# Optimization experiments

Measured on AMD Instinct MI355X. Metric: run time of the kernel, lower is better.

Reference implementation:

```python
import jax, jax.numpy as jnp
import numpy as np

EPS = 1e-6
START, END, FACTOR = 2.0, 8.0, 0.5


def layer_norm(x, w, b):
    mu = jnp.mean(x, axis=-1, keepdims=True)
    var = jnp.mean(jnp.square(x - mu), axis=-1, keepdims=True)
    return (x - mu) * jax.lax.rsqrt(var + EPS) * w + b


def build_spread_vector(hsize):
    # decay_i = factor ** (1 / k_i), k_i linearly spaced in [start, end]
    return FACTOR ** (1.0 / jnp.linspace(START, END, hsize, dtype=jnp.float32))


def decay_scan(decay, u):
    # cx[t] = decay * cx[t-1] + u[t], along axis 1 (seq). decay: [H], u: [B,S,H]
    a = jnp.broadcast_to(decay, u.shape)

    def combine(c1, c2):
        a1, b1 = c1
        a2, b2 = c2
        return a1 * a2, a2 * b1 + b2

    _, cx = jax.lax.associative_scan(combine, (a, u), axis=1)
    return cx


def setup_inputs() -> dict:
    key = jax.random.key(0)
    ks = jax.random.split(key, 4)
    B, S, D = 8, 2048, 1024
    sd = 1.0 / np.sqrt(D)
    return {
        "x": jax.random.normal(ks[0], (B, S, D), jnp.float32),
        "Wt": jax.random.normal(ks[1], (D, D), jnp.float32) * sd,
        "Wo": jax.random.normal(ks[2], (D, D), jnp.float32) * sd,
        "Wg": jax.random.normal(ks[3], (2 * D, D), jnp.float32) * sd,
        "bg": jnp.zeros((D,), jnp.float32),
        "ln1_w": jnp.ones((D,), jnp.float32),
        "ln1_b": jnp.zeros((D,), jnp.float32),
        "lnc_w": jnp.ones((D,), jnp.float32),
        "lnc_b": jnp.zeros((D,), jnp.float32),
        "lng_w": jnp.ones((D,), jnp.float32),
        "lng_b": jnp.zeros((D,), jnp.float32),
    }


def reference(x, Wt, Wo, Wg, bg, ln1_w, ln1_b, lnc_w, lnc_b, lng_w, lng_b):
    H = Wt.shape[1]
    decay = build_spread_vector(H)            # [H]
    decay_beta = 1.0 - decay
    _x = layer_norm(x, ln1_w, ln1_b)          # [B,S,D]
    u = jnp.einsum("bsd,dh->bsh", _x, Wt) * decay_beta
    cx = decay_scan(decay, u)                 # [B,S,H]
    out = jnp.einsum("bsh,hd->bsd", layer_norm(cx, lnc_w, lnc_b), Wo)
    res = _x                                  # norm_residual=True
    gate = jax.nn.sigmoid(
        layer_norm(jnp.concatenate((res, out), axis=-1) @ Wg + bg, lng_w, lng_b)
    )
    return (1.0 - gate) * res + gate * out
```

## Files before the change

### kernel.cpp

```cpp
#include <hip/hip_runtime.h>
#include <hip/hip_bf16.h>
#include <cmath>
#include <cstdint>

namespace {

constexpr int kB = 8;
constexpr int kS = 2048;
constexpr int kD = 1024;
constexpr int kN = kB * kS;
constexpr int kChunk = 32;
constexpr int kNChunk = kS / kChunk;
constexpr float kEps = 1e-6f;

typedef __attribute__((ext_vector_type(8))) short bf16x8;
typedef __attribute__((ext_vector_type(4))) float f32x4;

__device__ inline float bf2f(short s) {
  union { unsigned u; float f; } c;
  c.u = ((unsigned)(unsigned short)s) << 16;
  return c.f;
}

struct bh4 { __hip_bfloat16 a, b, c, d; };

__device__ inline void gload16(const void* g, void* l) {
  __builtin_amdgcn_global_load_lds(
      (const __attribute__((address_space(1))) void*)g,
      (__attribute__((address_space(3))) void*)l, 16, 0, 0);
}

__device__ inline void blockReduce2(float& s1, float& s2) {
#pragma unroll
  for (int off = 32; off > 0; off >>= 1) {
    s1 += __shfl_down(s1, off);
    s2 += __shfl_down(s2, off);
  }
  __shared__ float r1[4], r2[4];
  int wid = threadIdx.x >> 6;
  if ((threadIdx.x & 63) == 0) { r1[wid] = s1; r2[wid] = s2; }
  __syncthreads();
  s1 = r1[0] + r1[1] + r1[2] + r1[3];
  s2 = r2[0] + r2[1] + r2[2] + r2[3];
  __syncthreads();
}

__global__ __launch_bounds__(256) void k_prep_ln(
    const float* __restrict__ x, const float* __restrict__ ln1w,
    const float* __restrict__ ln1b, __hip_bfloat16* __restrict__ xnb,
    const float* __restrict__ Wt, const float* __restrict__ Wo,
    const float* __restrict__ Wg, __hip_bfloat16* __restrict__ WtT,
    __hip_bfloat16* __restrict__ WoT, __hip_bfloat16* __restrict__ WgT,
    float* __restrict__ decay, float* __restrict__ dbeta,
    float* __restrict__ aL) {
  int b = blockIdx.x;
  int t = threadIdx.x;
  if (b < kN) {
    int row = b;
    const float4 v = reinterpret_cast<const float4*>(x + (size_t)row * kD)[t];
    float s1 = v.x + v.y + v.z + v.w;
    float s2 = v.x * v.x + v.y * v.y + v.z * v.z + v.w * v.w;
    blockReduce2(s1, s2);
    float mu = s1 * (1.0f / kD);
    float var = s2 * (1.0f / kD) - mu * mu;
    float rs = rsqrtf(var + kEps);
    float4 wv = reinterpret_cast<const float4*>(ln1w)[t];
    float4 bv = reinterpret_cast<const float4*>(ln1b)[t];
    bh4 o;
    o.a = __float2bfloat16((v.x - mu) * rs * wv.x + bv.x);
    o.b = __float2bfloat16((v.y - mu) * rs * wv.y + bv.y);
    o.c = __float2bfloat16((v.z - mu) * rs * wv.z + bv.z);
    o.d = __float2bfloat16((v.w - mu) * rs * wv.w + bv.w);
    reinterpret_cast<bh4*>(xnb + (size_t)row * kD)[t] = o;
    return;
  }
  b -= kN;
  if (b < 4) {
    int h = b * 256 + t;
    float kk = 2.0f + 6.0f * (float)h / (float)(kD - 1);
    float d = exp2f(-1.0f / kk);
    decay[h] = d;
    dbeta[h] = 1.0f - d;
    aL[h] = exp2f(-(float)kChunk / kk);
    return;
  }
  b -= 4;
  const float* W;
  __hip_bfloat16* WT;
  int K, local;
  if (b < 1024)      { W = Wt; WT = WtT; K = kD;     local = b; }
  else if (b < 2048) { W = Wo; WT = WoT; K = kD;     local = b - 1024; }
  else               { W = Wg; WT = WgT; K = 2 * kD; local = b - 2048; }
  int n0 = (local & 31) * 32, k0 = (local >> 5) * 32;
  __shared__ float tile[32][33];
  int tr = t >> 3, tc4 = (t & 7) * 4;
  float4 v = *reinterpret_cast<const float4*>(W + (size_t)(k0 + tr) * kD + n0 + tc4);
  tile[tc4 + 0][tr] = v.x;
  tile[tc4 + 1][tr] = v.y;
  tile[tc4 + 2][tr] = v.z;
  tile[tc4 + 3][tr] = v.w;
  __syncthreads();
  bh4 o;
  o.a = __float2bfloat16(tile[tr][tc4 + 0]);
  o.b = __float2bfloat16(tile[tr][tc4 + 1]);
  o.c = __float2bfloat16(tile[tr][tc4 + 2]);
  o.d = __float2bfloat16(tile[tr][tc4 + 3]);
  *reinterpret_cast<bh4*>(WT + (size_t)(n0 + tr) * K + k0 + tc4) = o;
}

__global__ __launch_bounds__(512, 2) void k_mfma_gemm(
    const __hip_bfloat16* __restrict__ A1, const __hip_bfloat16* __restrict__ A2,
    const __hip_bfloat16* __restrict__ BT, int K,
    float* __restrict__ C, __hip_bfloat16* __restrict__ Cb,
    const float* __restrict__ colscale, const float* __restrict__ bias,
    float* __restrict__ ends, const float* __restrict__ decay) {
  __shared__ short As[2][2][8192];
  __shared__ short Bs[2][2][8192];
  const int t = threadIdx.x;
  const int wid = t >> 6, lane = t & 63;
  const int nwg = gridDim.x;
  const int bid = blockIdx.x;
  const int s = (bid & 7) * (nwg >> 3) + (bid >> 3);
  const int bn = (s & 3) * 256;
  const int bm = (s >> 2) * 256;
  const int wr = wid >> 2;
  const int wcn = wid & 3;
  const int r = lane & 15, kg = lane >> 4;
  const int NT = K / 64;

  const int srow = lane >> 3;
  const int scol = (((lane & 7) ^ srow)) * 8;

  auto stageA = [&](int kt, int h) {
    const __hip_bfloat16* Asrc = A1;
    int kk = kt * 64;
    if (A2 && kk >= kD) { Asrc = A2; kk -= kD; }
    short* dst = &As[kt & 1][h][0];
#pragma unroll
    for (int j = 0; j < 2; ++j) {
      int chunk = wid * 2 + j;
      int row = chunk * 8 + srow;
      gload16(Asrc + (size_t)(bm + h * 128 + row) * kD + kk + scol,
              dst + chunk * 512 + lane * 8);
    }
  };
  auto stageB = [&](int kt, int h) {
    short* dst = &Bs[kt & 1][h][0];
#pragma unroll
    for (int j = 0; j < 2; ++j) {
      int chunk = wid * 2 + j;
      int row = chunk * 8 + srow;
      gload16(BT + (size_t)(bn + h * 128 + row) * K + kt * 64 + scol,
              dst + chunk * 512 + lane * 8);
    }
  };

  f32x4 acc[8][4];
#pragma unroll
  for (int m = 0; m < 8; ++m)
#pragma unroll
    for (int n = 0; n < 4; ++n) acc[m][n] = (f32x4){0.f, 0.f, 0.f, 0.f};

  stageA(0, 0); stageA(0, 1); stageB(0, 0); stageB(0, 1);
  stageB(1, 0); stageB(1, 1);
  asm volatile("s_waitcnt vmcnt(4)" ::: "memory");
  __builtin_amdgcn_s_barrier();
  asm volatile("" ::: "memory");

  for (int T = 0; T < NT; ++T) {
    const int bc = T & 1;
    const char* Ab = reinterpret_cast<const char*>(&As[bc][wr][0]);
    const char* Bb = reinterpret_cast<const char*>(&Bs[bc][wcn >> 1][0]);
    const int bcol = (wcn & 1) * 64;
    bf16x8 bfr[4][2], aLO[4][2], aHI[4][2];
#pragma unroll
    for (int n = 0; n < 4; ++n)
#pragma unroll
      for (int ks = 0; ks < 2; ++ks) {
        int row = bcol + n * 16 + r;
        int slot = (ks * 4 + kg) ^ (r & 7);
        bfr[n][ks] = *reinterpret_cast<const bf16x8*>(Bb + row * 128 + slot * 16);
      }
#pragma unroll
    for (int mm = 0; mm < 4; ++mm)
#pragma unroll
      for (int ks = 0; ks < 2; ++ks) {
        int row = mm * 16 + r;
        int slot = (ks * 4 + kg) ^ (r & 7);
        aLO[mm][ks] = *reinterpret_cast<const bf16x8*>(Ab + row * 128 + slot * 16);
      }
    if (T + 1 < NT) { stageA(T + 1, 0); stageA(T + 1, 1); }
    asm volatile("" ::: "memory");
    __builtin_amdgcn_s_barrier();
    asm volatile("" ::: "memory");
    __builtin_amdgcn_s_setprio(1);
#pragma unroll
    for (int mm = 0; mm < 4; ++mm)
#pragma unroll
      for (int n = 0; n < 4; ++n)
#pragma unroll
        for (int ks = 0; ks < 2; ++ks)
          acc[mm][n] = __builtin_amdgcn_mfma_f32_16x16x32_bf16(
              aLO[mm][ks], bfr[n][ks], acc[mm][n], 0, 0, 0);
    __builtin_amdgcn_s_setprio(0);
    asm volatile("" ::: "memory");
    __builtin_amdgcn_s_barrier();
    asm volatile("" ::: "memory");
#pragma unroll
    for (int mm = 0; mm < 4; ++mm)
#pragma unroll
      for (int ks = 0; ks < 2; ++ks) {
        int row = (mm + 4) * 16 + r;
        int slot = (ks * 4 + kg) ^ (r & 7);
        aHI[mm][ks] = *reinterpret_cast<const bf16x8*>(Ab + row * 128 + slot * 16);
      }
    if (T + 2 < NT) { stageB(T + 2, 0); stageB(T + 2, 1); }
    asm volatile("" ::: "memory");
    __builtin_amdgcn_s_barrier();
    asm volatile("" ::: "memory");
    __builtin_amdgcn_s_setprio(1);
#pragma unroll
    for (int mm = 0; mm < 4; ++mm)
#pragma unroll
      for (int n = 0; n < 4; ++n)
#pragma unroll
        for (int ks = 0; ks < 2; ++ks)
          acc[mm + 4][n] = __builtin_amdgcn_mfma_f32_16x16x32_bf16(
              aHI[mm][ks], bfr[n][ks], acc[mm + 4][n], 0, 0, 0);
    __builtin_amdgcn_s_setprio(0);
    if (T + 2 < NT)
      asm volatile("s_waitcnt vmcnt(4)" ::: "memory");
    else if (T + 1 < NT)
      asm volatile("s_waitcnt vmcnt(0)" ::: "memory");
    asm volatile("" ::: "memory");
    __builtin_amdgcn_s_barrier();
    asm volatile("" ::: "memory");
  }

  int col[4];
  float cs[4], bi[4];
#pragma unroll
  for (int n = 0; n < 4; ++n) {
    col[n] = bn + wcn * 64 + n * 16 + r;
    cs[n] = colscale ? colscale[col[n]] : 1.0f;
    bi[n] = bias ? bias[col[n]] : 0.0f;
  }
#pragma unroll
  for (int m = 0; m < 8; ++m) {
#pragma unroll
    for (int j = 0; j < 4; ++j) {
      int row = bm + wr * 128 + m * 16 + kg * 4 + j;
#pragma unroll
      for (int n = 0; n < 4; ++n) {
        float v = acc[m][n][j] * cs[n] + bi[n];
        if (C) C[(size_t)row * kD + col[n]] = v;
        if (Cb) Cb[(size_t)row * kD + col[n]] = __float2bfloat16(v);
      }
    }
  }

  if (ends) {
    const int row0 = bm + wr * 128;
    const int chunk0 = row0 >> 5;
#pragma unroll
    for (int n = 0; n < 4; ++n) {
      float a = decay[col[n]];
      float a2 = a * a, a4 = a2 * a2, a8 = a4 * a4, a16 = a8 * a8;
      float pw = (kg == 3) ? 1.0f
               : (kg == 2) ? a4
               : (kg == 1) ? a4 * a4
                           : a4 * a4 * a4;
      float v3 = pw, v2 = pw * a, v1 = pw * a2, v0 = pw * a2 * a;
      const float vj[4] = {v0, v1, v2, v3};
#pragma unroll
      for (int c2 = 0; c2 < 4; ++c2) {
        float p = 0.f;
#pragma unroll
        for (int j = 0; j < 4; ++j) {
          float u0 = acc[2 * c2][n][j] * cs[n] + bi[n];
          float u1 = acc[2 * c2 + 1][n][j] * cs[n] + bi[n];
          p += vj[j] * (a16 * u0 + u1);
        }
        p += __shfl_xor(p, 16);
        p += __shfl_xor(p, 32);
        if (kg == 0) ends[(size_t)(chunk0 + c2) * kD + col[n]] = p;
      }
    }
  }
}

__global__ __launch_bounds__(256) void k_scan_carry(
    const float* __restrict__ ends, const float* __restrict__ aL,
    float* __restrict__ carry) {
  int tid = blockIdx.x * blockDim.x + threadIdx.x;
  int h = tid & (kD - 1);
  int b = tid >> 10;
  float al = aL[h];
  float car = 0.f;
#pragma unroll
  for (int c = 0; c < kNChunk; ++c) {
    size_t idx = ((size_t)(b * kNChunk + c)) * kD + h;
    carry[idx] = car;
    car = fmaf(al, car, ends[idx]);
  }
}

__global__ __launch_bounds__(256) void k_scan_apply_ln(
    const __hip_bfloat16* __restrict__ u, const float* __restrict__ decay,
    const float* __restrict__ carry, const float* __restrict__ lnw,
    const float* __restrict__ lnb, __hip_bfloat16* __restrict__ cxn) {
  const int blk = blockIdx.x;
  const int t = threadIdx.x;
  const int h0 = t * 4;
  const int b = blk >> 6, c = blk & 63;
  const size_t rowbase = (size_t)b * kS + (size_t)c * kChunk;

  float a0 = decay[h0], a1 = decay[h0 + 1], a2 = decay[h0 + 2],
        a3 = decay[h0 + 3];
  const float4 cv = *reinterpret_cast<const float4*>(
      carry + (size_t)blk * kD + h0);
  float v0 = cv.x, v1 = cv.y, v2 = cv.z, v3 = cv.w;
  const float4 wv = *reinterpret_cast<const float4*>(lnw + h0);
  const float4 bv = *reinterpret_cast<const float4*>(lnb + h0);

  for (int i = 0; i < kChunk; ++i) {
    short4 q = *reinterpret_cast<const short4*>(u + (rowbase + i) * kD + h0);
    v0 = fmaf(a0, v0, bf2f(q.x));
    v1 = fmaf(a1, v1, bf2f(q.y));
    v2 = fmaf(a2, v2, bf2f(q.z));
    v3 = fmaf(a3, v3, bf2f(q.w));
    float s1 = v0 + v1 + v2 + v3;
    float s2 = v0 * v0 + v1 * v1 + v2 * v2 + v3 * v3;
    blockReduce2(s1, s2);
    float mu = s1 * (1.0f / kD);
    float var = s2 * (1.0f / kD) - mu * mu;
    float rs = rsqrtf(var + kEps);
    bh4 o;
    o.a = __float2bfloat16((v0 - mu) * rs * wv.x + bv.x);
    o.b = __float2bfloat16((v1 - mu) * rs * wv.y + bv.y);
    o.c = __float2bfloat16((v2 - mu) * rs * wv.z + bv.z);
    o.d = __float2bfloat16((v3 - mu) * rs * wv.w + bv.w);
    *reinterpret_cast<bh4*>(cxn + (rowbase + i) * kD + h0) = o;
  }
}

__global__ __launch_bounds__(256) void k_final(
    const __hip_bfloat16* __restrict__ gpre, const __hip_bfloat16* __restrict__ res,
    const __hip_bfloat16* __restrict__ outp, const float* __restrict__ w,
    const float* __restrict__ b, float* __restrict__ y) {
  int row = blockIdx.x;
  int t = threadIdx.x;
  short4 q = reinterpret_cast<const short4*>(gpre + (size_t)row * kD)[t];
  float vv[4] = {bf2f(q.x), bf2f(q.y), bf2f(q.z), bf2f(q.w)};
  float s1 = vv[0] + vv[1] + vv[2] + vv[3];
  float s2 = vv[0] * vv[0] + vv[1] * vv[1] + vv[2] * vv[2] + vv[3] * vv[3];
  blockReduce2(s1, s2);
  float mu = s1 * (1.0f / kD);
  float var = s2 * (1.0f / kD) - mu * mu;
  float rs = rsqrtf(var + kEps);
  float4 wv = reinterpret_cast<const float4*>(w)[t];
  float4 bv = reinterpret_cast<const float4*>(b)[t];
  short4 r4 = reinterpret_cast<const short4*>(res + (size_t)row * kD)[t];
  short4 o4 = reinterpret_cast<const short4*>(outp + (size_t)row * kD)[t];
  float rr[4] = {bf2f(r4.x), bf2f(r4.y), bf2f(r4.z), bf2f(r4.w)};
  float oo[4] = {bf2f(o4.x), bf2f(o4.y), bf2f(o4.z), bf2f(o4.w)};
  float ww[4] = {wv.x, wv.y, wv.z, wv.w};
  float bb[4] = {bv.x, bv.y, bv.z, bv.w};
  float4 out;
  float* op = &out.x;
#pragma unroll
  for (int i = 0; i < 4; ++i) {
    float z = (vv[i] - mu) * rs * ww[i] + bb[i];
    float g = 1.0f / (1.0f + expf(-z));
    op[i] = rr[i] + g * (oo[i] - rr[i]);
  }
  reinterpret_cast<float4*>(y + (size_t)row * kD)[t] = out;
}

}

extern "C" void kernel_launch(void* const* d_in, const int* in_sizes, int n_in,
                              void* d_out, int out_size, void* d_ws,
                              size_t ws_size, hipStream_t stream) {
  const float* x = (const float*)d_in[0];
  const float* Wt = (const float*)d_in[1];
  const float* Wo = (const float*)d_in[2];
  const float* Wg = (const float*)d_in[3];
  const float* bg = (const float*)d_in[4];
  const float* ln1w = (const float*)d_in[5];
  const float* ln1b = (const float*)d_in[6];
  const float* lncw = (const float*)d_in[7];
  const float* lncb = (const float*)d_in[8];
  const float* lngw = (const float*)d_in[9];
  const float* lngb = (const float*)d_in[10];
  float* y = (float*)d_out;

  char* ws = (char*)d_ws;
  size_t off = 0;
  auto alloc = [&](size_t bytes) {
    char* p = ws + off;
    off += (bytes + 255) & ~(size_t)255;
    return p;
  };
  __hip_bfloat16* xnb = (__hip_bfloat16*)alloc((size_t)kN * kD * 2);
  __hip_bfloat16* ub = (__hip_bfloat16*)alloc((size_t)kN * kD * 2);
  __hip_bfloat16* outb = (__hip_bfloat16*)alloc((size_t)kN * kD * 2);
  __hip_bfloat16* cxn = (__hip_bfloat16*)alloc((size_t)kN * kD * 2);
  __hip_bfloat16* WtT = (__hip_bfloat16*)alloc((size_t)kD * kD * 2);
  __hip_bfloat16* WoT = (__hip_bfloat16*)alloc((size_t)kD * kD * 2);
  __hip_bfloat16* WgT = (__hip_bfloat16*)alloc((size_t)kD * 2 * kD * 2);
  float* decay = (float*)alloc(kD * 4);
  float* dbeta = (float*)alloc(kD * 4);
  float* aL = (float*)alloc(kD * 4);
  float* ends = (float*)alloc((size_t)kB * kNChunk * kD * 4);
  float* carry = (float*)alloc((size_t)kB * kNChunk * kD * 4);

  const int nwg = (kD / 256) * (kN / 256);

  k_prep_ln<<<kN + 4 + 4096, 256, 0, stream>>>(
      x, ln1w, ln1b, xnb, Wt, Wo, Wg, WtT, WoT, WgT, decay, dbeta, aL);
  k_mfma_gemm<<<nwg, 512, 0, stream>>>(xnb, nullptr, WtT, kD, nullptr, ub,
                                       dbeta, nullptr, ends, decay);
  k_scan_carry<<<(kB * kD) / 256, 256, 0, stream>>>(ends, aL, carry);
  k_scan_apply_ln<<<kB * kNChunk, 256, 0, stream>>>(ub, decay, carry, lncw,
                                                    lncb, cxn);
  k_mfma_gemm<<<nwg, 512, 0, stream>>>(cxn, nullptr, WoT, kD, nullptr, outb,
                                       nullptr, nullptr, nullptr, nullptr);
  k_mfma_gemm<<<nwg, 512, 0, stream>>>(xnb, outb, WgT, 2 * kD, nullptr, ub,
                                       nullptr, bg, nullptr, nullptr);
  k_final<<<kN, 256, 0, stream>>>(ub, xnb, outb, lngw, lngb, y);
}
```

Measured before the change: 225.8 us.

## Stage scan chunk in LDS and compute per-row LayerNorm stats after scan

The scan-apply kernel used to do a full block reduction with two barriers for every one of the 32 rows in a chunk. It now writes the scanned values as bf16 into padded shared memory and computes all 32 rows' mean and variance at once, with 8 threads per row using wavefront shuffles. A final pass then normalizes from LDS. This removes most block barriers, but the LayerNorm statistics are now computed on bf16-rounded values. The trailing barrier in blockReduce2 is also removed, which risks a race on its shared scratch when it is called repeatedly.

```diff
diff --git a/kernel.cpp b/kernel.cpp
--- a/kernel.cpp
+++ b/kernel.cpp
@@ -42,7 +42,6 @@
   __syncthreads();
   s1 = r1[0] + r1[1] + r1[2] + r1[3];
   s2 = r2[0] + r2[1] + r2[2] + r2[3];
-  __syncthreads();
 }
 
 __global__ __launch_bounds__(256) void k_prep_ln(
@@ -309,38 +308,76 @@
     const __hip_bfloat16* __restrict__ u, const float* __restrict__ decay,
     const float* __restrict__ carry, const float* __restrict__ lnw,
     const float* __restrict__ lnb, __hip_bfloat16* __restrict__ cxn) {
+  constexpr int PADH = kD + 8;
+  __shared__ short cxs[kChunk * PADH];
+  __shared__ float smu[kChunk], srs[kChunk];
   const int blk = blockIdx.x;
   const int t = threadIdx.x;
   const int h0 = t * 4;
   const int b = blk >> 6, c = blk & 63;
   const size_t rowbase = (size_t)b * kS + (size_t)c * kChunk;
 
-  float a0 = decay[h0], a1 = decay[h0 + 1], a2 = decay[h0 + 2],
-        a3 = decay[h0 + 3];
-  const float4 cv = *reinterpret_cast<const float4*>(
-      carry + (size_t)blk * kD + h0);
-  float v0 = cv.x, v1 = cv.y, v2 = cv.z, v3 = cv.w;
-  const float4 wv = *reinterpret_cast<const float4*>(lnw + h0);
-  const float4 bv = *reinterpret_cast<const float4*>(lnb + h0);
-
-  for (int i = 0; i < kChunk; ++i) {
-    short4 q = *reinterpret_cast<const short4*>(u + (rowbase + i) * kD + h0);
-    v0 = fmaf(a0, v0, bf2f(q.x));
-    v1 = fmaf(a1, v1, bf2f(q.y));
-    v2 = fmaf(a2, v2, bf2f(q.z));
-    v3 = fmaf(a3, v3, bf2f(q.w));
-    float s1 = v0 + v1 + v2 + v3;
-    float s2 = v0 * v0 + v1 * v1 + v2 * v2 + v3 * v3;
-    blockReduce2(s1, s2);
-    float mu = s1 * (1.0f / kD);
-    float var = s2 * (1.0f / kD) - mu * mu;
-    float rs = rsqrtf(var + kEps);
-    bh4 o;
-    o.a = __float2bfloat16((v0 - mu) * rs * wv.x + bv.x);
-    o.b = __float2bfloat16((v1 - mu) * rs * wv.y + bv.y);
-    o.c = __float2bfloat16((v2 - mu) * rs * wv.z + bv.z);
-    o.d = __float2bfloat16((v3 - mu) * rs * wv.w + bv.w);
-    *reinterpret_cast<bh4*>(cxn + (rowbase + i) * kD + h0) = o;
+  {
+    float a0 = decay[h0], a1 = decay[h0 + 1], a2 = decay[h0 + 2],
+          a3 = decay[h0 + 3];
+    const float4 cv = *reinterpret_cast<const float4*>(
+        carry + (size_t)blk * kD + h0);
+    float v0 = cv.x, v1 = cv.y, v2 = cv.z, v3 = cv.w;
+#pragma unroll 4
+    for (int i = 0; i < kChunk; ++i) {
+      short4 q = *reinterpret_cast<const short4*>(u + (rowbase + i) * kD + h0);
+      v0 = fmaf(a0, v0, bf2f(q.x));
+      v1 = fmaf(a1, v1, bf2f(q.y));
+      v2 = fmaf(a2, v2, bf2f(q.z));
+      v3 = fmaf(a3, v3, bf2f(q.w));
+      bh4 o;
+      o.a = __float2bfloat16(v0);
+      o.b = __float2bfloat16(v1);
+      o.c = __float2bfloat16(v2);
+      o.d = __float2bfloat16(v3);
+      *reinterpret_cast<bh4*>(&cxs[i * PADH + h0]) = o;
+    }
+  }
+  __syncthreads();
+  {
+    int row = t >> 3, j = t & 7;
+    float s1 = 0.f, s2 = 0.f;
+#pragma unroll
+    for (int ch = 0; ch < 16; ++ch) {
+      bf16x8 vv = *reinterpret_cast<const bf16x8*>(
+          &cxs[row * PADH + j * 128 + ch * 8]);
+#pragma unroll
+      for (int e = 0; e < 8; ++e) {
+        float f = bf2f(vv[e]);
+        s1 += f;
+        s2 += f * f;
+      }
+    }
+    s1 += __shfl_xor(s1, 1); s2 += __shfl_xor(s2, 1);
+    s1 += __shfl_xor(s1, 2); s2 += __shfl_xor(s2, 2);
+    s1 += __shfl_xor(s1, 4); s2 += __shfl_xor(s2, 4);
+    if (j == 0) {
+      float mu = s1 * (1.0f / kD);
+      float var = s2 * (1.0f / kD) - mu * mu;
+      smu[row] = mu;
+      srs[row] = rsqrtf(var + kEps);
+    }
+  }
+  __syncthreads();
+  {
+    const float4 wv = *reinterpret_cast<const float4*>(lnw + h0);
+    const float4 bv = *reinterpret_cast<const float4*>(lnb + h0);
+#pragma unroll 4
+    for (int i = 0; i < kChunk; ++i) {
+      short4 q = *reinterpret_cast<const short4*>(&cxs[i * PADH + h0]);
+      float mu = smu[i], rs = srs[i];
+      bh4 o;
+      o.a = __float2bfloat16((bf2f(q.x) - mu) * rs * wv.x + bv.x);
+      o.b = __float2bfloat16((bf2f(q.y) - mu) * rs * wv.y + bv.y);
+      o.c = __float2bfloat16((bf2f(q.z) - mu) * rs * wv.z + bv.z);
+      o.d = __float2bfloat16((bf2f(q.w) - mu) * rs * wv.w + bv.w);
+      *reinterpret_cast<bh4*>(cxn + (rowbase + i) * kD + h0) = o;
+    }
   }
 }
 
```

After: 219.6 us, median of 2. -2.7%, faster.
